# Performance work log

Hardware: AMD Instinct MI355X
Metric: run time of the kernel (lower is better)

## Reference

```python
import jax, jax.numpy as jnp
import numpy as np

N_NODES = 50000
N_EDGES = 800000
IN_CH = 128
HID_CH = 128


def glorot(key, shape):
    fan_in, fan_out = shape[0], shape[1]
    lim = np.sqrt(6.0 / (fan_in + fan_out)).astype(np.float32)
    return jax.random.uniform(key, shape, jnp.float32, -lim, lim)


def setup_inputs() -> dict:
    key = jax.random.key(0)
    k1, k2, k3, k4 = jax.random.split(key, 4)
    x = jax.random.normal(k1, (N_NODES, IN_CH), jnp.float32)
    edge_index = jax.random.randint(k2, (2, N_EDGES), 0, N_NODES, jnp.int64)
    W1 = glorot(k3, (IN_CH, HID_CH))
    b1 = jnp.zeros((HID_CH,), jnp.float32)
    W2 = glorot(k4, (HID_CH, HID_CH))
    b2 = jnp.zeros((HID_CH,), jnp.float32)
    return {"x": x, "edge_index": edge_index, "W1": W1, "b1": b1, "W2": W2, "b2": b2}


def _gcn_conv(x, W, b, src, dst, n_nodes):
    # PyG GCNConv: h = D^{-1/2} (A + I) D^{-1/2} (x W) + b
    h = x @ W  # [N, H] transform first (as in PyG)
    loops = jnp.arange(n_nodes, dtype=src.dtype)
    s = jnp.concatenate([src, loops])  # add self-loops
    d = jnp.concatenate([dst, loops])
    deg = jnp.zeros((n_nodes,), h.dtype).at[d].add(1.0)
    dinv = jnp.where(deg > 0, jax.lax.rsqrt(deg), 0.0)
    coef = dinv[s] * dinv[d]  # [E+N]
    msg = h[s] * coef[:, None]  # gather + scale
    out = jax.ops.segment_sum(msg, d, num_segments=n_nodes)  # scatter-add
    return out + b


def reference(x, edge_index, W1, b1, W2, b2):
    src, dst = edge_index[0], edge_index[1]
    n = x.shape[0]
    h = jax.nn.relu(_gcn_conv(x, W1, b1, src, dst, n))
    h = jax.nn.relu(_gcn_conv(h, W2, b2, src, dst, n))
    return h
```

## Files before the change

### kernel.cpp

```cpp
#include <hip/hip_runtime.h>

#define N_NODES 50000
#define N_EDGES 800000
#define CH 128
#define NBUCK 196
#define B_BIN 250
#define CHUNK 3200
#define G_GEMM 782

typedef __attribute__((ext_vector_type(8))) short bf16x8;
typedef __attribute__((ext_vector_type(4))) float f32x4;

__device__ __forceinline__ float bf2f(unsigned short u) {
    union { unsigned int i; float f; } c;
    c.i = ((unsigned int)u) << 16;
    return c.f;
}
__device__ __forceinline__ unsigned short f2bf(float f) {
    union { float f; unsigned int i; } c;
    c.f = f;
    unsigned int lsb = (c.i >> 16) & 1u;
    c.i += 0x7fffu + lsb;
    return (unsigned short)(c.i >> 16);
}

__global__ __launch_bounds__(256) void k_wt(const float* __restrict__ Wa,
                                            const float* __restrict__ Wb,
                                            unsigned short* __restrict__ Wta,
                                            unsigned short* __restrict__ Wtb) {
    const float* W = blockIdx.x ? Wb : Wa;
    unsigned short* Wt = blockIdx.x ? Wtb : Wta;
    const int tid = threadIdx.x;
    for (int i = 0; i < 64; ++i) {
        int idx = i * 256 + tid;
        int n = idx >> 7, kk = idx & 127;
        Wt[idx] = f2bf(W[kk * CH + n]);
    }
}

__global__ __launch_bounds__(256) void k_mega(
        const int* __restrict__ ei, int* __restrict__ blk_base,
        const float* __restrict__ X, const unsigned short* __restrict__ Wt1,
        unsigned short* __restrict__ HS1u) {
    const int tid = threadIdx.x;
    const int b = blockIdx.x;

    if (b < B_BIN) {
        __shared__ int h[NBUCK];
        for (int i = tid; i < NBUCK; i += 256) h[i] = 0;
        __syncthreads();
        const int e0 = b * CHUNK;
        const int* dst = ei + N_EDGES;
        for (int i = tid; i < CHUNK; i += 256)
            atomicAdd(&h[dst[e0 + i] >> 8], 1);
        __syncthreads();
        for (int k = tid; k < NBUCK; k += 256)
            blk_base[b * NBUCK + k] = h[k];
        return;
    }

    const int gb = b - B_BIN;
    const int l = tid & 63, w = tid >> 6;
    const int lm = l & 15, lk = l >> 4;
    const int row0 = gb * 64 + w * 16;

    int arow = row0 + lm;
    if (arow >= N_NODES) arow = N_NODES - 1;
    bf16x8 a[4];
    #pragma unroll
    for (int ki = 0; ki < 4; ++ki) {
        const float* ap = &X[arow * CH + ki * 32 + lk * 8];
        float4 f0 = *(const float4*)ap;
        float4 f1 = *(const float4*)(ap + 4);
        bf16x8 af;
        af[0] = (short)f2bf(f0.x); af[1] = (short)f2bf(f0.y);
        af[2] = (short)f2bf(f0.z); af[3] = (short)f2bf(f0.w);
        af[4] = (short)f2bf(f1.x); af[5] = (short)f2bf(f1.y);
        af[6] = (short)f2bf(f1.z); af[7] = (short)f2bf(f1.w);
        a[ki] = af;
    }

    #pragma unroll
    for (int ct = 0; ct < 8; ++ct) {
        const unsigned short* wp = &Wt1[(ct * 16 + lm) * CH + lk * 8];
        f32x4 acc = {0.f, 0.f, 0.f, 0.f};
        #pragma unroll
        for (int ki = 0; ki < 4; ++ki) {
            bf16x8 bfrag = *(const bf16x8*)&wp[ki * 32];
            acc = __builtin_amdgcn_mfma_f32_16x16x32_bf16(a[ki], bfrag, acc, 0, 0, 0);
        }
        #pragma unroll
        for (int r = 0; r < 4; ++r) {
            int row = row0 + lk * 4 + r;
            if (row < N_NODES)
                HS1u[row * CH + ct * 16 + lm] = f2bf(acc[r]);
        }
    }
}

__global__ __launch_bounds__(256) void k_colscan(int* __restrict__ blk_base,
                                                 int* __restrict__ bucket_cnt) {
    __shared__ int sm[256];
    const int tid = threadIdx.x, k = blockIdx.x;
    int v = (tid < B_BIN) ? blk_base[tid * NBUCK + k] : 0;
    sm[tid] = v;
    __syncthreads();
    #pragma unroll
    for (int off = 1; off < 256; off <<= 1) {
        int t = (tid >= off) ? sm[tid - off] : 0;
        __syncthreads();
        sm[tid] += t;
        __syncthreads();
    }
    if (tid < B_BIN) blk_base[tid * NBUCK + k] = sm[tid] - v;
    if (tid == 255) bucket_cnt[k] = sm[255];
}

__global__ __launch_bounds__(256) void k_bin_place(const int* __restrict__ ei,
                                                   const int* __restrict__ bucket_cnt,
                                                   const int* __restrict__ blk_base,
                                                   unsigned int* __restrict__ ebuf) {
    __shared__ int sm[256];
    __shared__ int bbase[NBUCK];
    __shared__ int h[NBUCK];
    const int tid = threadIdx.x, b = blockIdx.x;

    int v = (tid < NBUCK) ? bucket_cnt[tid] : 0;
    sm[tid] = v;
    __syncthreads();
    #pragma unroll
    for (int off = 1; off < 256; off <<= 1) {
        int t = (tid >= off) ? sm[tid - off] : 0;
        __syncthreads();
        sm[tid] += t;
        __syncthreads();
    }
    if (tid < NBUCK) bbase[tid] = sm[tid] - v;
    for (int i = tid; i < NBUCK; i += 256) h[i] = 0;
    __syncthreads();

    const int e0 = b * CHUNK;
    for (int i = tid; i < CHUNK; i += 256) {
        int s = ei[e0 + i];
        int d = ei[N_EDGES + e0 + i];
        int k = d >> 8;
        int loc = atomicAdd(&h[k], 1);
        int pos = bbase[k] + blk_base[b * NBUCK + k] + loc;
        ebuf[pos] = ((unsigned int)s << 8) | (unsigned int)(d & 255);
    }
}

__global__ __launch_bounds__(256) void k_bucket_csr(const unsigned int* __restrict__ ebuf,
                                                    const int* __restrict__ bucket_cnt,
                                                    int* __restrict__ rowptr,
                                                    int* __restrict__ col,
                                                    float* __restrict__ dinv,
                                                    unsigned short* __restrict__ HS1u) {
    __shared__ int cnts[256];
    __shared__ int fillc[256];
    __shared__ int sm[256];
    __shared__ float sdinv[256];
    __shared__ int e0s;
    const int tid = threadIdx.x, k = blockIdx.x;
    const int node0 = k << 8;

    int vb = (tid < NBUCK) ? bucket_cnt[tid] : 0;
    sm[tid] = vb;
    __syncthreads();
    #pragma unroll
    for (int off = 1; off < 256; off <<= 1) {
        int t = (tid >= off) ? sm[tid - off] : 0;
        __syncthreads();
        sm[tid] += t;
        __syncthreads();
    }
    if (tid == k) e0s = sm[tid] - vb;
    cnts[tid] = 0;
    __syncthreads();
    const int e0 = e0s;
    const int cnt = bucket_cnt[k];

    for (int i = tid; i < cnt; i += 256)
        atomicAdd(&cnts[ebuf[e0 + i] & 255], 1);
    __syncthreads();

    int v = cnts[tid];
    sm[tid] = v;
    __syncthreads();
    #pragma unroll
    for (int off = 1; off < 256; off <<= 1) {
        int t = (tid >= off) ? sm[tid - off] : 0;
        __syncthreads();
        sm[tid] += t;
        __syncthreads();
    }
    int rp = sm[tid] - v;
    fillc[tid] = rp;
    float dval = rsqrtf((float)(v + 1));
    sdinv[tid] = dval;
    int node = node0 + tid;
    if (node < N_NODES) {
        rowptr[node] = e0 + rp;
        dinv[node] = dval;
    }
    if (k == NBUCK - 1 && tid == 0) rowptr[N_NODES] = N_EDGES;
    __syncthreads();

    for (int i = tid; i < cnt; i += 256) {
        unsigned int pv = ebuf[e0 + i];
        int j = pv & 255;
        int loc = atomicAdd(&fillc[j], 1);
        col[e0 + loc] = (int)(pv >> 8);
    }

    ushort4* H4 = (ushort4*)HS1u;
    #pragma unroll 4
    for (int t = 0; t < 32; ++t) {
        int u = t * 256 + tid;
        int r = u >> 5, c = u & 31;
        int nd = node0 + r;
        if (nd < N_NODES) {
            ushort4 v4 = H4[nd * 32 + c];
            float sc = sdinv[r];
            v4.x = f2bf(bf2f(v4.x) * sc);
            v4.y = f2bf(bf2f(v4.y) * sc);
            v4.z = f2bf(bf2f(v4.z) * sc);
            v4.w = f2bf(bf2f(v4.w) * sc);
            H4[nd * 32 + c] = v4;
        }
    }
}

__global__ __launch_bounds__(256) void k_agg_gemm(
        const int* __restrict__ rowptr, const int* __restrict__ col,
        const unsigned short* __restrict__ HS1, const float* __restrict__ dinv,
        const float* __restrict__ b1, const unsigned short* __restrict__ Wt2,
        unsigned short* __restrict__ HS2) {
    __shared__ __align__(16) unsigned short hl[64 * 136];
    const int tid = threadIdx.x;
    const int node0 = blockIdx.x * 64;
    const int lane = tid & 31;
    const ushort4* H4 = (const ushort4*)HS1;

    float4 bb = *(const float4*)&b1[lane * 4];

    #pragma unroll 2
    for (int pass = 0; pass < 8; ++pass) {
        int nl = pass * 8 + (tid >> 5);
        int node = node0 + nl;
        if (node < N_NODES) {
            int e0 = rowptr[node];
            int e1 = rowptr[node + 1];
            float dd = dinv[node];

            ushort4 hv = H4[node * 32 + lane];
            float ax = bf2f(hv.x), ay = bf2f(hv.y), az = bf2f(hv.z), aw = bf2f(hv.w);

            int e = e0;
            for (; e + 3 < e1; e += 4) {
                int s0 = col[e], s1 = col[e + 1], s2 = col[e + 2], s3 = col[e + 3];
                ushort4 v0 = H4[s0 * 32 + lane];
                ushort4 v1 = H4[s1 * 32 + lane];
                ushort4 v2 = H4[s2 * 32 + lane];
                ushort4 v3 = H4[s3 * 32 + lane];
                ax += (bf2f(v0.x) + bf2f(v1.x)) + (bf2f(v2.x) + bf2f(v3.x));
                ay += (bf2f(v0.y) + bf2f(v1.y)) + (bf2f(v2.y) + bf2f(v3.y));
                az += (bf2f(v0.z) + bf2f(v1.z)) + (bf2f(v2.z) + bf2f(v3.z));
                aw += (bf2f(v0.w) + bf2f(v1.w)) + (bf2f(v2.w) + bf2f(v3.w));
            }
            for (; e < e1; ++e) {
                ushort4 va = H4[col[e] * 32 + lane];
                ax += bf2f(va.x); ay += bf2f(va.y); az += bf2f(va.z); aw += bf2f(va.w);
            }

            ushort4 o;
            o.x = f2bf(fmaxf(ax * dd + bb.x, 0.f));
            o.y = f2bf(fmaxf(ay * dd + bb.y, 0.f));
            o.z = f2bf(fmaxf(az * dd + bb.z, 0.f));
            o.w = f2bf(fmaxf(aw * dd + bb.w, 0.f));
            *(ushort4*)&hl[nl * 136 + lane * 4] = o;
        }
    }
    __syncthreads();

    const int l = tid & 63, w = tid >> 6;
    const int lm = l & 15, lk = l >> 4;
    const int row0 = node0 + w * 16;

    bf16x8 a[4];
    #pragma unroll
    for (int ki = 0; ki < 4; ++ki)
        a[ki] = *(const bf16x8*)&hl[(w * 16 + lm) * 136 + ki * 32 + lk * 8];

    #pragma unroll
    for (int ct = 0; ct < 8; ++ct) {
        const unsigned short* wp = &Wt2[(ct * 16 + lm) * CH + lk * 8];
        f32x4 acc = {0.f, 0.f, 0.f, 0.f};
        #pragma unroll
        for (int ki = 0; ki < 4; ++ki) {
            bf16x8 bfrag = *(const bf16x8*)&wp[ki * 32];
            acc = __builtin_amdgcn_mfma_f32_16x16x32_bf16(a[ki], bfrag, acc, 0, 0, 0);
        }
        #pragma unroll
        for (int r = 0; r < 4; ++r) {
            int row = row0 + lk * 4 + r;
            if (row < N_NODES)
                HS2[row * CH + ct * 16 + lm] = f2bf(acc[r] * dinv[row]);
        }
    }
}

__global__ __launch_bounds__(256) void k_agg_final(
        const int* __restrict__ rowptr, const int* __restrict__ col,
        const unsigned short* __restrict__ HS, const float* __restrict__ dinv,
        const float* __restrict__ b, float* __restrict__ OUT) {
    int gid = blockIdx.x * 256 + threadIdx.x;
    int node = gid >> 5;
    if (node >= N_NODES) return;
    int lane = gid & 31;
    const ushort4* H4 = (const ushort4*)HS;

    int e0 = rowptr[node];
    int e1 = rowptr[node + 1];

    ushort4 hself = H4[node * 32 + lane];
    float ax = bf2f(hself.x), ay = bf2f(hself.y), az = bf2f(hself.z), aw = bf2f(hself.w);

    int e = e0;
    for (; e + 3 < e1; e += 4) {
        int s0 = col[e], s1 = col[e + 1], s2 = col[e + 2], s3 = col[e + 3];
        ushort4 v0 = H4[s0 * 32 + lane];
        ushort4 v1 = H4[s1 * 32 + lane];
        ushort4 v2 = H4[s2 * 32 + lane];
        ushort4 v3 = H4[s3 * 32 + lane];
        ax += (bf2f(v0.x) + bf2f(v1.x)) + (bf2f(v2.x) + bf2f(v3.x));
        ay += (bf2f(v0.y) + bf2f(v1.y)) + (bf2f(v2.y) + bf2f(v3.y));
        az += (bf2f(v0.z) + bf2f(v1.z)) + (bf2f(v2.z) + bf2f(v3.z));
        aw += (bf2f(v0.w) + bf2f(v1.w)) + (bf2f(v2.w) + bf2f(v3.w));
    }
    for (; e < e1; ++e) {
        ushort4 va = H4[col[e] * 32 + lane];
        ax += bf2f(va.x); ay += bf2f(va.y); az += bf2f(va.z); aw += bf2f(va.w);
    }

    float di = dinv[node];
    float4 bb = *(const float4*)&b[lane * 4];
    float4 o;
    o.x = fmaxf(ax * di + bb.x, 0.f);
    o.y = fmaxf(ay * di + bb.y, 0.f);
    o.z = fmaxf(az * di + bb.z, 0.f);
    o.w = fmaxf(aw * di + bb.w, 0.f);
    *(float4*)&OUT[node * CH + lane * 4] = o;
}

extern "C" void kernel_launch(void* const* d_in, const int* in_sizes, int n_in,
                              void* d_out, int out_size, void* d_ws, size_t ws_size,
                              hipStream_t stream) {
    const float* x  = (const float*)d_in[0];
    const int*   ei = (const int*)d_in[1];
    const float* W1 = (const float*)d_in[2];
    const float* b1 = (const float*)d_in[3];
    const float* W2 = (const float*)d_in[4];
    const float* b2 = (const float*)d_in[5];
    float* out = (float*)d_out;

    int* blk_base    = (int*)d_ws;
    int* bucket_cnt  = blk_base + 49152;
    int* rowptr      = bucket_cnt + 256;
    int* col         = rowptr + 50176;
    float* dinv      = (float*)(col + 800256);
    unsigned int* ebuf = (unsigned int*)(dinv + 50176);
    unsigned short* hs1 = (unsigned short*)(ebuf + 800256);
    unsigned short* hs2  = hs1 + 6400000;
    unsigned short* wt1  = hs2 + 6400000;
    unsigned short* wt2  = wt1 + 16384;

    const int gA = (N_NODES * 32 + 255) / 256;

    k_wt<<<2, 256, 0, stream>>>(W1, W2, wt1, wt2);
    k_mega<<<B_BIN + G_GEMM, 256, 0, stream>>>(ei, blk_base, x, wt1, hs1);
    k_colscan<<<NBUCK, 256, 0, stream>>>(blk_base, bucket_cnt);
    k_bin_place<<<B_BIN, 256, 0, stream>>>(ei, bucket_cnt, blk_base, ebuf);
    k_bucket_csr<<<NBUCK, 256, 0, stream>>>(ebuf, bucket_cnt, rowptr, col, dinv, hs1);
    k_agg_gemm<<<G_GEMM, 256, 0, stream>>>(rowptr, col, hs1, dinv, b1, wt2, hs2);
    k_agg_final<<<gA, 256, 0, stream>>>(rowptr, col, hs2, dinv, b2, out);
}
```

Measured before the change: 168.8 us.

## Reorder layer-2 as aggregate-then-transform and split fused agg+GEMM into kernels

Layer 2 now aggregates first and applies the W2 GEMM afterwards, using associativity of A(hW). The first aggregation kernel applies bias, ReLU and a pre-scale by dinv, and a second aggregation produces the normalized A·h. A standalone MFMA GEMM then adds b2, applies ReLU and writes fp32 output. The aggregation kernels use 16 lanes per node with 16-byte loads, replacing 32 lanes with 8-byte loads. In exchange this adds a kernel launch and an extra bf16 intermediate buffer round-trip through memory.

```diff
diff --git a/kernel.cpp b/kernel.cpp
--- a/kernel.cpp
+++ b/kernel.cpp
@@ -9,6 +9,7 @@
 #define G_GEMM 782
 
 typedef __attribute__((ext_vector_type(8))) short bf16x8;
+typedef __attribute__((ext_vector_type(8))) unsigned short u16x8;
 typedef __attribute__((ext_vector_type(4))) float f32x4;
 
 __device__ __forceinline__ float bf2f(unsigned short u) {
@@ -231,66 +232,75 @@
     }
 }
 
-__global__ __launch_bounds__(256) void k_agg_gemm(
+template <int MODE>
+__global__ __launch_bounds__(256) void k_agg(
         const int* __restrict__ rowptr, const int* __restrict__ col,
-        const unsigned short* __restrict__ HS1, const float* __restrict__ dinv,
-        const float* __restrict__ b1, const unsigned short* __restrict__ Wt2,
-        unsigned short* __restrict__ HS2) {
-    __shared__ __align__(16) unsigned short hl[64 * 136];
+        const unsigned short* __restrict__ H, const float* __restrict__ dinv,
+        const float* __restrict__ b, unsigned short* __restrict__ OUT) {
+    int gid = blockIdx.x * 256 + threadIdx.x;
+    int node = gid >> 4;
+    if (node >= N_NODES) return;
+    int lane = gid & 15;
+    const u16x8* H8 = (const u16x8*)H;
+
+    int e0 = rowptr[node];
+    int e1 = rowptr[node + 1];
+
+    u16x8 hv = H8[node * 16 + lane];
+    float acc[8];
+    #pragma unroll
+    for (int j = 0; j < 8; ++j) acc[j] = bf2f(hv[j]);
+
+    int e = e0;
+    for (; e + 3 < e1; e += 4) {
+        int s0 = col[e], s1 = col[e + 1], s2 = col[e + 2], s3 = col[e + 3];
+        u16x8 v0 = H8[s0 * 16 + lane];
+        u16x8 v1 = H8[s1 * 16 + lane];
+        u16x8 v2 = H8[s2 * 16 + lane];
+        u16x8 v3 = H8[s3 * 16 + lane];
+        #pragma unroll
+        for (int j = 0; j < 8; ++j)
+            acc[j] += (bf2f(v0[j]) + bf2f(v1[j])) + (bf2f(v2[j]) + bf2f(v3[j]));
+    }
+    for (; e < e1; ++e) {
+        u16x8 v = H8[col[e] * 16 + lane];
+        #pragma unroll
+        for (int j = 0; j < 8; ++j) acc[j] += bf2f(v[j]);
+    }
+
+    float di = dinv[node];
+    u16x8 o;
+    if (MODE == 0) {
+        float4 b0 = *(const float4*)&b[lane * 8];
+        float4 b1v = *(const float4*)&b[lane * 8 + 4];
+        float bb[8] = {b0.x, b0.y, b0.z, b0.w, b1v.x, b1v.y, b1v.z, b1v.w};
+        #pragma unroll
+        for (int j = 0; j < 8; ++j)
+            o[j] = f2bf(fmaxf(acc[j] * di + bb[j], 0.f) * di);
+    } else {
+        #pragma unroll
+        for (int j = 0; j < 8; ++j)
+            o[j] = f2bf(acc[j] * di);
+    }
+    *(u16x8*)&OUT[node * CH + lane * 8] = o;
+}
+
+__global__ __launch_bounds__(256) void k_gemm_out(
+        const unsigned short* __restrict__ A2,
+        const unsigned short* __restrict__ Wt2,
+        const float* __restrict__ b2,
+        float* __restrict__ OUT) {
     const int tid = threadIdx.x;
-    const int node0 = blockIdx.x * 64;
-    const int lane = tid & 31;
-    const ushort4* H4 = (const ushort4*)HS1;
-
-    float4 bb = *(const float4*)&b1[lane * 4];
-
-    #pragma unroll 2
-    for (int pass = 0; pass < 8; ++pass) {
-        int nl = pass * 8 + (tid >> 5);
-        int node = node0 + nl;
-        if (node < N_NODES) {
-            int e0 = rowptr[node];
-            int e1 = rowptr[node + 1];
-            float dd = dinv[node];
-
-            ushort4 hv = H4[node * 32 + lane];
-            float ax = bf2f(hv.x), ay = bf2f(hv.y), az = bf2f(hv.z), aw = bf2f(hv.w);
-
-            int e = e0;
-            for (; e + 3 < e1; e += 4) {
-                int s0 = col[e], s1 = col[e + 1], s2 = col[e + 2], s3 = col[e + 3];
-                ushort4 v0 = H4[s0 * 32 + lane];
-                ushort4 v1 = H4[s1 * 32 + lane];
-                ushort4 v2 = H4[s2 * 32 + lane];
-                ushort4 v3 = H4[s3 * 32 + lane];
-                ax += (bf2f(v0.x) + bf2f(v1.x)) + (bf2f(v2.x) + bf2f(v3.x));
-                ay += (bf2f(v0.y) + bf2f(v1.y)) + (bf2f(v2.y) + bf2f(v3.y));
-                az += (bf2f(v0.z) + bf2f(v1.z)) + (bf2f(v2.z) + bf2f(v3.z));
-                aw += (bf2f(v0.w) + bf2f(v1.w)) + (bf2f(v2.w) + bf2f(v3.w));
-            }
-            for (; e < e1; ++e) {
-                ushort4 va = H4[col[e] * 32 + lane];
-                ax += bf2f(va.x); ay += bf2f(va.y); az += bf2f(va.z); aw += bf2f(va.w);
-            }
-
-            ushort4 o;
-            o.x = f2bf(fmaxf(ax * dd + bb.x, 0.f));
-            o.y = f2bf(fmaxf(ay * dd + bb.y, 0.f));
-            o.z = f2bf(fmaxf(az * dd + bb.z, 0.f));
-            o.w = f2bf(fmaxf(aw * dd + bb.w, 0.f));
-            *(ushort4*)&hl[nl * 136 + lane * 4] = o;
-        }
-    }
-    __syncthreads();
-
     const int l = tid & 63, w = tid >> 6;
     const int lm = l & 15, lk = l >> 4;
-    const int row0 = node0 + w * 16;
-
+    const int row0 = blockIdx.x * 64 + w * 16;
+
+    int arow = row0 + lm;
+    if (arow >= N_NODES) arow = N_NODES - 1;
     bf16x8 a[4];
     #pragma unroll
     for (int ki = 0; ki < 4; ++ki)
-        a[ki] = *(const bf16x8*)&hl[(w * 16 + lm) * 136 + ki * 32 + lk * 8];
+        a[ki] = *(const bf16x8*)&A2[arow * CH + ki * 32 + lk * 8];
 
     #pragma unroll
     for (int ct = 0; ct < 8; ++ct) {
@@ -301,56 +311,14 @@
             bf16x8 bfrag = *(const bf16x8*)&wp[ki * 32];
             acc = __builtin_amdgcn_mfma_f32_16x16x32_bf16(a[ki], bfrag, acc, 0, 0, 0);
         }
+        float bb = b2[ct * 16 + lm];
         #pragma unroll
         for (int r = 0; r < 4; ++r) {
             int row = row0 + lk * 4 + r;
             if (row < N_NODES)
-                HS2[row * CH + ct * 16 + lm] = f2bf(acc[r] * dinv[row]);
-        }
-    }
-}
-
-__global__ __launch_bounds__(256) void k_agg_final(
-        const int* __restrict__ rowptr, const int* __restrict__ col,
-        const unsigned short* __restrict__ HS, const float* __restrict__ dinv,
-        const float* __restrict__ b, float* __restrict__ OUT) {
-    int gid = blockIdx.x * 256 + threadIdx.x;
-    int node = gid >> 5;
-    if (node >= N_NODES) return;
-    int lane = gid & 31;
-    const ushort4* H4 = (const ushort4*)HS;
-
-    int e0 = rowptr[node];
-    int e1 = rowptr[node + 1];
-
-    ushort4 hself = H4[node * 32 + lane];
-    float ax = bf2f(hself.x), ay = bf2f(hself.y), az = bf2f(hself.z), aw = bf2f(hself.w);
-
-    int e = e0;
-    for (; e + 3 < e1; e += 4) {
-        int s0 = col[e], s1 = col[e + 1], s2 = col[e + 2], s3 = col[e + 3];
-        ushort4 v0 = H4[s0 * 32 + lane];
-        ushort4 v1 = H4[s1 * 32 + lane];
-        ushort4 v2 = H4[s2 * 32 + lane];
-        ushort4 v3 = H4[s3 * 32 + lane];
-        ax += (bf2f(v0.x) + bf2f(v1.x)) + (bf2f(v2.x) + bf2f(v3.x));
-        ay += (bf2f(v0.y) + bf2f(v1.y)) + (bf2f(v2.y) + bf2f(v3.y));
-        az += (bf2f(v0.z) + bf2f(v1.z)) + (bf2f(v2.z) + bf2f(v3.z));
-        aw += (bf2f(v0.w) + bf2f(v1.w)) + (bf2f(v2.w) + bf2f(v3.w));
-    }
-    for (; e < e1; ++e) {
-        ushort4 va = H4[col[e] * 32 + lane];
-        ax += bf2f(va.x); ay += bf2f(va.y); az += bf2f(va.z); aw += bf2f(va.w);
-    }
-
-    float di = dinv[node];
-    float4 bb = *(const float4*)&b[lane * 4];
-    float4 o;
-    o.x = fmaxf(ax * di + bb.x, 0.f);
-    o.y = fmaxf(ay * di + bb.y, 0.f);
-    o.z = fmaxf(az * di + bb.z, 0.f);
-    o.w = fmaxf(aw * di + bb.w, 0.f);
-    *(float4*)&OUT[node * CH + lane * 4] = o;
+                OUT[row * CH + ct * 16 + lm] = fmaxf(acc[r] + bb, 0.f);
+        }
+    }
 }
 
 extern "C" void kernel_launch(void* const* d_in, const int* in_sizes, int n_in,
@@ -371,17 +339,19 @@
     float* dinv      = (float*)(col + 800256);
     unsigned int* ebuf = (unsigned int*)(dinv + 50176);
     unsigned short* hs1 = (unsigned short*)(ebuf + 800256);
-    unsigned short* hs2  = hs1 + 6400000;
-    unsigned short* wt1  = hs2 + 6400000;
-    unsigned short* wt2  = wt1 + 16384;
-
-    const int gA = (N_NODES * 32 + 255) / 256;
+    unsigned short* h1p = hs1 + 6400000;
+    unsigned short* a2  = h1p + 6400000;
+    unsigned short* wt1 = a2 + 6400000;
+    unsigned short* wt2 = wt1 + 16384;
+
+    const int gAgg = 3125;
 
     k_wt<<<2, 256, 0, stream>>>(W1, W2, wt1, wt2);
     k_mega<<<B_BIN + G_GEMM, 256, 0, stream>>>(ei, blk_base, x, wt1, hs1);
     k_colscan<<<NBUCK, 256, 0, stream>>>(blk_base, bucket_cnt);
     k_bin_place<<<B_BIN, 256, 0, stream>>>(ei, bucket_cnt, blk_base, ebuf);
     k_bucket_csr<<<NBUCK, 256, 0, stream>>>(ebuf, bucket_cnt, rowptr, col, dinv, hs1);
-    k_agg_gemm<<<G_GEMM, 256, 0, stream>>>(rowptr, col, hs1, dinv, b1, wt2, hs2);
-    k_agg_final<<<gA, 256, 0, stream>>>(rowptr, col, hs2, dinv, b2, out);
-}
+    k_agg<0><<<gAgg, 256, 0, stream>>>(rowptr, col, hs1, dinv, b1, h1p);
+    k_agg<1><<<gAgg, 256, 0, stream>>>(rowptr, col, h1p, dinv, nullptr, a2);
+    k_gemm_out<<<G_GEMM, 256, 0, stream>>>(a2, wt2, b2, out);
+}
```

Result: faster. 152.6 us (-9.6%).
